# Optimization experiments

Hardware: AMD Instinct MI355X
Metric: run time of the kernel (lower is better)

Reference implementation:

```python
import jax, jax.numpy as jnp
import numpy as np

L, E, D, H, HD, DFF = 15, 1024, 1024, 32, 32, 1536
SC, SH, SG, SEQ, B = 32, 256, 256, 64, 128
ALPHA = (2.0 * L) ** (-0.25)


def setup_inputs() -> dict:
    keys = iter(jax.random.split(jax.random.key(0), 40))
    def rn(shape, s=0.02):
        return jax.random.normal(next(keys), shape, jnp.float32) * s
    inp = {"x": jax.random.normal(next(keys), (B, SEQ, E), jnp.float32)}
    inp.update(
        wq_w=rn((L, E, D)), wq_b=rn((L, D)),
        wk_w=rn((L, E, D)), wk_b=rn((L, D)),
        wv_w=rn((L, E, D)), wv_b=rn((L, D)),
        wo_w=rn((L, D, E)), wo_b=rn((L, E)),
        sc_w=rn((L, E, SC)),
        sh1_w=rn((L, SEQ * SC, SH)), sh1_b=rn((L, SH)),
        sln1_g=jnp.ones((L, SH)), sln1_b=jnp.zeros((L, SH)),
        sgf_w=rn((L, SH, H * SG)), sgf_b=rn((L, H * SG)),
        sln2_g=jnp.ones((L, H * SG)), sln2_b=jnp.zeros((L, H * SG)),
        swg_w=rn((L, SG, SEQ * SEQ)),
        ffn1_w=rn((L, E, DFF)), ffn1_b=rn((L, DFF)),
        ffn2_w=rn((L, DFF, E)), ffn2_b=rn((L, E)),
        n1_g=jnp.ones((L, E)), n1_b=jnp.zeros((L, E)),
        n2_g=jnp.ones((L, E)), n2_b=jnp.zeros((L, E)),
    )
    return inp


def _ln(x, g, b, eps=1e-3):
    m = jnp.mean(x, -1, keepdims=True)
    v = jnp.mean((x - m) ** 2, -1, keepdims=True)
    return (x - m) * jax.lax.rsqrt(v + eps) * g + b


def _mish(x):
    return x * jnp.tanh(jax.nn.softplus(x))


def _encoder_layer(x, p):
    (wq_w, wq_b, wk_w, wk_b, wv_w, wv_b, wo_w, wo_b, sc_w, sh1_w, sh1_b,
     sln1_g, sln1_b, sgf_w, sgf_b, sln2_g, sln2_b, swg_w,
     ffn1_w, ffn1_b, ffn2_w, ffn2_b, n1_g, n1_b, n2_g, n2_b) = p
    b, l, _ = x.shape
    q = (x @ wq_w + wq_b).reshape(b, l, H, HD)
    k = (x @ wk_w + wk_b).reshape(b, l, H, HD)
    v = (x @ wv_w + wv_b).reshape(b, l, H, HD)
    logits = jnp.einsum('bqhd,bkhd->bhqk', q, k) / jnp.sqrt(jnp.float32(HD))
    # smolgen: dynamic per-head 64x64 bias from compressed board features
    c = (x @ sc_w).reshape(b, l * SC)                       # [B, 2048]
    h = _ln(jax.nn.silu(c @ sh1_w + sh1_b), sln1_g, sln1_b)  # [B, 256]
    g = _ln(jax.nn.silu(h @ sgf_w + sgf_b), sln2_g, sln2_b)  # [B, H*256]
    sw = (g.reshape(b, H, SG) @ swg_w).reshape(b, H, l, l)   # [B, H, 64, 64]
    attn = jax.nn.softmax(logits + sw, axis=-1)
    av = jnp.einsum('bhqk,bkhd->bqhd', attn, v).reshape(b, l, D)
    out1 = _ln(x + (av @ wo_w + wo_b) * ALPHA, n1_g, n1_b)
    f = _mish(out1 @ ffn1_w + ffn1_b) @ ffn2_w + ffn2_b
    return _ln(out1 + f * ALPHA, n2_g, n2_b)


def reference(x, wq_w, wq_b, wk_w, wk_b, wv_w, wv_b, wo_w, wo_b, sc_w,
              sh1_w, sh1_b, sln1_g, sln1_b, sgf_w, sgf_b, sln2_g, sln2_b,
              swg_w, ffn1_w, ffn1_b, ffn2_w, ffn2_b, n1_g, n1_b, n2_g, n2_b):
    params = (wq_w, wq_b, wk_w, wk_b, wv_w, wv_b, wo_w, wo_b, sc_w,
              sh1_w, sh1_b, sln1_g, sln1_b, sgf_w, sgf_b, sln2_g, sln2_b,
              swg_w, ffn1_w, ffn1_b, ffn2_w, ffn2_b, n1_g, n1_b, n2_g, n2_b)
    def body(h, p):
        return _encoder_layer(h, p), None
    out, _ = jax.lax.scan(body, x, params)
    return out
```

## Files before the change

### kernel.cpp

```cpp
#include <hip/hip_runtime.h>
#include <hip/hip_bf16.h>

typedef __attribute__((ext_vector_type(8))) short bf16x8;
typedef __attribute__((ext_vector_type(4))) float f32x4;
typedef __hip_bfloat16 bf16;

#define ALPHA_F 0.42728713f
#define LN_EPS 1e-3f

__device__ __forceinline__ float silu_f(float x) { return x / (1.0f + __expf(-x)); }
__device__ __forceinline__ float mish_f(float x) {
  if (x > 20.0f) return x;
  float t = 1.0f + __expf(x);
  float t2 = t * t;
  return x * (t2 - 1.0f) / (t2 + 1.0f);
}
__device__ __forceinline__ unsigned short f2bfu(float x) {
  bf16 h = __float2bfloat16(x);
  return *(unsigned short*)&h;
}
__device__ __forceinline__ float bfu2f(unsigned short u) {
  unsigned int v = (unsigned int)u << 16;
  return *(float*)&v;
}

#define MFMA16(acc, a, b) \
  (acc) = __builtin_amdgcn_mfma_f32_16x16x32_bf16((a), (b), (acc), 0, 0, 0)

#define GLOAD_LDS16(gp, lp)                                                              \
  __builtin_amdgcn_global_load_lds((__attribute__((address_space(1))) void*)(void*)(gp), \
                                   (__attribute__((address_space(3))) void*)(void*)(lp), \
                                   16, 0, 0)

__global__ __launch_bounds__(1) void sentinel_k(float* __restrict__ o) { o[0] = 1.2345e7f; }

__device__ __forceinline__ void transpose_body(
    int tb, float* tile ,
    const float* wq, const float* wk, const float* wv, const float* wo,
    const float* f1, const float* f2, const float* sgf, const float* swg,
    const float* sh1, const float* scw,
    const float* bq, const float* bk, const float* bv,
    bf16* Wqkv, bf16* Wo, bf16* Wf1, bf16* Wf2, bf16* Wsgf, bf16* Wswg,
    bf16* Wsh1, bf16* Wsc, float* bqkv) {
  if (tb >= 10784) {
    int i = (tb - 10784) * 256 + threadIdx.x;
    if (i < 1024) bqkv[i] = bq[i];
    else if (i < 2048) bqkv[i] = bk[i - 1024];
    else bqkv[i] = bv[i - 2048];
    return;
  }
  const float* W;
  bf16* Wt;
  int K, N, b2;
  if (tb < 3072) {
    int m = tb >> 10;
    W = (m == 0) ? wq : ((m == 1) ? wk : wv);
    Wt = Wqkv + (size_t)m * 1024 * 1024;
    K = 1024; N = 1024; b2 = tb & 1023;
  } else if (tb < 4096)  { W = wo;  Wt = Wo;   K = 1024; N = 1024; b2 = tb - 3072; }
  else if (tb < 5632)    { W = f1;  Wt = Wf1;  K = 1024; N = 1536; b2 = tb - 4096; }
  else if (tb < 7168)    { W = f2;  Wt = Wf2;  K = 1536; N = 1024; b2 = tb - 5632; }
  else if (tb < 9216)    { W = sgf; Wt = Wsgf; K = 256;  N = 8192; b2 = tb - 7168; }
  else if (tb < 10240)   { W = swg; Wt = Wswg; K = 256;  N = 4096; b2 = tb - 9216; }
  else if (tb < 10752)   { W = sh1; Wt = Wsh1; K = 2048; N = 256;  b2 = tb - 10240; }
  else                   { W = scw; Wt = Wsc;  K = 1024; N = 32;   b2 = tb - 10752; }
  int ntx = N >> 5;
  int ty_ = b2 / ntx, tx_ = b2 - ty_ * ntx;
  int nb = tx_ * 32, kb = ty_ * 32;
  int tx = threadIdx.x & 31, ty = threadIdx.x >> 5;
#pragma unroll
  for (int i = 0; i < 4; ++i)
    tile[(ty + i * 8) * 33 + tx] = W[(size_t)(kb + ty + i * 8) * N + nb + tx];
  __syncthreads();
#pragma unroll
  for (int i = 0; i < 4; ++i)
    Wt[(size_t)(nb + ty + i * 8) * K + kb + tx] = __float2bfloat16(tile[tx * 33 + ty + i * 8]);
}

__global__ __launch_bounds__(256) void transpose_layer(
    const float* wq, const float* wk, const float* wv, const float* wo,
    const float* f1, const float* f2, const float* sgf, const float* swg,
    const float* sh1, const float* scw,
    const float* bq, const float* bk, const float* bv,
    bf16* Wqkv, bf16* Wo, bf16* Wf1, bf16* Wf2, bf16* Wsgf, bf16* Wswg,
    bf16* Wsh1, bf16* Wsc, float* bqkv) {
  __shared__ float tile[32 * 33];
  transpose_body(blockIdx.x, tile, wq, wk, wv, wo, f1, f2, sgf, swg, sh1, scw,
                 bq, bk, bv, Wqkv, Wo, Wf1, Wf2, Wsgf, Wswg, Wsh1, Wsc, bqkv);
}

__global__ __launch_bounds__(256) void cvt_f32_bf16_k(const float* __restrict__ in,
                                                      bf16* __restrict__ out, long long n) {
  long long i = ((long long)blockIdx.x * 256 + threadIdx.x) * 4;
  if (i + 3 < n) {
    float4 v = *(const float4*)(in + i);
    out[i + 0] = __float2bfloat16(v.x);
    out[i + 1] = __float2bfloat16(v.y);
    out[i + 2] = __float2bfloat16(v.z);
    out[i + 3] = __float2bfloat16(v.w);
  }
}

__global__ __launch_bounds__(256) void megaA(
    const bf16* __restrict__ xb,
    const bf16* __restrict__ Wqkv, const float* __restrict__ bqkv,
    bf16* __restrict__ qkvb,
    const bf16* __restrict__ Wsc, bf16* __restrict__ cbuf,
    int doT,
    const float* wq, const float* wk, const float* wv, const float* wo,
    const float* f1, const float* f2, const float* sgf, const float* swg,
    const float* sh1, const float* scw,
    const float* bq, const float* bk, const float* bv,
    bf16* WqkvN, bf16* WoN, bf16* Wf1N, bf16* Wf2N, bf16* WsgfN, bf16* WswgN,
    bf16* Wsh1N, bf16* WscN, float* bqkvN) {
  __shared__ __align__(128) short LB[16384];
  const int bid = blockIdx.x;
  const int t = threadIdx.x;
  if (bid < 1536) {
    const int lane = t & 63, wave = t >> 6;
    int xcd = bid & 7, lid = bid >> 3;
    int swz = xcd * 192 + lid;
    int by = swz / 24, bx = swz - by * 24;
    int m0 = by << 7, n0 = bx << 7;
    int wr = wave >> 1, wc = wave & 1;
    int fr = lane & 15, fk = (lane >> 4) << 3;
    f32x4 acc[4][4] = {};
    int row0 = t >> 2, ko0 = (t & 3) << 3;
    const bf16* Ag0 = xb + (size_t)(m0 + row0) * 1024 + ko0;
    const bf16* Ag1 = xb + (size_t)(m0 + 64 + row0) * 1024 + ko0;
    const bf16* Bg0 = Wqkv + (size_t)(n0 + row0) * 1024 + ko0;
    const bf16* Bg1 = Wqkv + (size_t)(n0 + 64 + row0) * 1024 + ko0;
    auto stageTo = [&](int buf, int k0) {
      short* Asb = LB + buf * 4096;
      short* Bsb = LB + 8192 + buf * 4096;
      GLOAD_LDS16(Ag0 + k0, Asb + wave * 512);
      GLOAD_LDS16(Ag1 + k0, Asb + 2048 + wave * 512);
      GLOAD_LDS16(Bg0 + k0, Bsb + wave * 512);
      GLOAD_LDS16(Bg1 + k0, Bsb + 2048 + wave * 512);
    };
    stageTo(0, 0);
    __syncthreads();
    const int rdA = (wr * 64 + fr) * 32 + fk;
    const int rdB = (wc * 64 + fr) * 32 + fk;
    for (int kt = 0; kt < 32; ++kt) {
      int cur = kt & 1;
      if (kt + 1 < 32) stageTo(cur ^ 1, (kt + 1) << 5);
      const short* Asb = LB + cur * 4096;
      const short* Bsb = LB + 8192 + cur * 4096;
      bf16x8 af[4], bfv[4];
#pragma unroll
      for (int a = 0; a < 4; ++a) af[a] = *(const bf16x8*)(Asb + rdA + a * 512);
#pragma unroll
      for (int b = 0; b < 4; ++b) bfv[b] = *(const bf16x8*)(Bsb + rdB + b * 512);
#pragma unroll
      for (int a = 0; a < 4; ++a)
#pragma unroll
        for (int b = 0; b < 4; ++b) MFMA16(acc[a][b], af[a], bfv[b]);
      __syncthreads();
    }
    int lr = (lane >> 4) << 2, lc = lane & 15;
#pragma unroll
    for (int a = 0; a < 4; ++a)
#pragma unroll
      for (int b = 0; b < 4; ++b) {
        int col = n0 + wc * 64 + b * 16 + lc;
        float bv = bqkv[col];
#pragma unroll
        for (int j = 0; j < 4; ++j) {
          int rowi = m0 + wr * 64 + a * 16 + lr + j;
          qkvb[(size_t)rowi * 3072 + col] = __float2bfloat16(acc[a][b][j] + bv);
        }
      }
  } else if (bid < 1664) {
    const int lane = t & 63, w = t >> 6;
    const int fr = lane & 15, s4 = lane >> 4;
    const int row0 = ((bid - 1536) * 4 + w) * 16;
    f32x4 acc[2] = {};
    const bf16* Arow = xb + (size_t)(row0 + fr) * 1024 + s4 * 8;
    const bf16* B0 = Wsc + (size_t)fr * 1024 + s4 * 8;
    const bf16* B1 = Wsc + (size_t)(16 + fr) * 1024 + s4 * 8;
#pragma unroll 8
    for (int kt = 0; kt < 32; ++kt) {
      bf16x8 a = *(const bf16x8*)(Arow + kt * 32);
      bf16x8 b0 = *(const bf16x8*)(B0 + kt * 32);
      bf16x8 b1 = *(const bf16x8*)(B1 + kt * 32);
      acc[0] = __builtin_amdgcn_mfma_f32_16x16x32_bf16(a, b0, acc[0], 0, 0, 0);
      acc[1] = __builtin_amdgcn_mfma_f32_16x16x32_bf16(a, b1, acc[1], 0, 0, 0);
    }
#pragma unroll
    for (int n2 = 0; n2 < 2; ++n2)
#pragma unroll
      for (int j = 0; j < 4; ++j)
        cbuf[(size_t)(row0 + s4 * 4 + j) * 32 + n2 * 16 + fr] =
            __float2bfloat16(acc[n2][j]);
  } else {
    if (!doT) return;
    transpose_body(bid - 1664, (float*)LB, wq, wk, wv, wo, f1, f2, sgf, swg, sh1, scw,
                   bq, bk, bv, WqkvN, WoN, Wf1N, Wf2N, WsgfN, WswgN, Wsh1N, WscN, bqkvN);
  }
}

template <int ACT, bool OUTBF16, bool BIAS>
__global__ __launch_bounds__(256) void gemm64b(const bf16* __restrict__ A,
                                               const bf16* __restrict__ Bt,
                                               const float* __restrict__ bias,
                                               float* __restrict__ Cf, bf16* __restrict__ Cb,
                                               int M, int N, int K) {
  __shared__ __align__(128) short As[2 * 4096];
  __shared__ __align__(128) short Bs[2 * 4096];
  int t = threadIdx.x;
  int lane = t & 63, wave = t >> 6;
  int nbx = N >> 6;
  int nwg = gridDim.x;
  int q = nwg >> 3, r = nwg & 7;
  int xcd = blockIdx.x & 7, lid = blockIdx.x >> 3;
  int swz = (xcd < r ? xcd * (q + 1) : r * (q + 1) + (xcd - r) * q) + lid;
  int by = swz / nbx, bx = swz - by * nbx;
  int m0 = by << 6, n0 = bx << 6;
  int fr = lane & 15;
  int fk = (lane >> 4) << 3;

  f32x4 acc[4] = {};

  int row0 = t >> 2, ko0 = (t & 3) << 3;
  const bf16* Ag0 = A + (size_t)(m0 + row0) * K + ko0;
  const bf16* Bg0 = Bt + (size_t)(n0 + row0) * K + ko0;

  auto stageTo = [&](int buf, int k0) {
#pragma unroll
    for (int s = 0; s < 2; ++s) {
      GLOAD_LDS16(Ag0 + k0 + s * 32, As + buf * 4096 + s * 2048 + wave * 512);
      GLOAD_LDS16(Bg0 + k0 + s * 32, Bs + buf * 4096 + s * 2048 + wave * 512);
    }
  };

  int nk = K >> 6;
  stageTo(0, 0);
  __syncthreads();

  const int rdA = (wave * 16 + fr) * 32 + fk;
  const int rdB = fr * 32 + fk;

  for (int kt = 0; kt < nk; ++kt) {
    int cur = kt & 1;
    if (kt + 1 < nk) stageTo(cur ^ 1, (kt + 1) << 6);
    bf16x8 af[2], bfv[4][2];
#pragma unroll
    for (int h = 0; h < 2; ++h) {
      af[h] = *(const bf16x8*)(As + cur * 4096 + h * 2048 + rdA);
#pragma unroll
      for (int b = 0; b < 4; ++b)
        bfv[b][h] = *(const bf16x8*)(Bs + cur * 4096 + h * 2048 + rdB + b * 512);
    }
#pragma unroll
    for (int h = 0; h < 2; ++h)
#pragma unroll
      for (int b = 0; b < 4; ++b) MFMA16(acc[b], af[h], bfv[b][h]);
    __syncthreads();
  }
  int lr = (lane >> 4) << 2;
  int lc = lane & 15;
#pragma unroll
  for (int b = 0; b < 4; ++b) {
    int col = n0 + b * 16 + lc;
    float bv = 0.0f;
    if constexpr (BIAS) bv = bias[col];
#pragma unroll
    for (int j = 0; j < 4; ++j) {
      int rowi = m0 + wave * 16 + lr + j;
      float v = acc[b][j] + bv;
      if constexpr (ACT == 1) v = silu_f(v);
      if constexpr (ACT == 2) v = mish_f(v);
      if constexpr (OUTBF16) Cb[(size_t)rowi * N + col] = __float2bfloat16(v);
      else Cf[(size_t)rowi * N + col] = v;
    }
  }
}

template <int ACT>
__global__ __launch_bounds__(64) void gemm_wave16(const bf16* __restrict__ A,
                                                  const bf16* __restrict__ Bt,
                                                  const float* __restrict__ bias,
                                                  float* __restrict__ Cf,
                                                  int N, int K) {
  const int lane = threadIdx.x;
  const int fr = lane & 15, s4 = lane >> 4;
  const int ncols = N >> 4;
  const int rb = blockIdx.x / ncols, cb = blockIdx.x - rb * ncols;
  const int row0 = rb << 4, col0 = cb << 4;
  f32x4 acc = {};
  const bf16* Arow = A + (size_t)(row0 + fr) * K + s4 * 8;
  const bf16* Brow = Bt + (size_t)(col0 + fr) * K + s4 * 8;
  const int nk = K >> 5;
#pragma unroll 8
  for (int kt = 0; kt < nk; ++kt) {
    bf16x8 a = *(const bf16x8*)(Arow + kt * 32);
    bf16x8 b = *(const bf16x8*)(Brow + kt * 32);
    acc = __builtin_amdgcn_mfma_f32_16x16x32_bf16(a, b, acc, 0, 0, 0);
  }
#pragma unroll
  for (int j = 0; j < 4; ++j) {
    int col = col0 + fr;
    float v = acc[j] + bias[col];
    if constexpr (ACT == 1) v = silu_f(v);
    Cf[(size_t)(row0 + s4 * 4 + j) * N + col] = v;
  }
}

__global__ __launch_bounds__(256) void ln256_kernel(const float* __restrict__ hpre,
                                                    const float* __restrict__ gam,
                                                    const float* __restrict__ bet,
                                                    bf16* __restrict__ hb) {
  __shared__ float rsm[4], rs2[4], st2[2];
  int t = threadIdx.x, row = blockIdx.x;
  float sv = hpre[(size_t)row * 256 + t];
  float s = sv, s2 = sv * sv;
#pragma unroll
  for (int o = 32; o > 0; o >>= 1) { s += __shfl_down(s, o); s2 += __shfl_down(s2, o); }
  if ((t & 63) == 0) { rsm[t >> 6] = s; rs2[t >> 6] = s2; }
  __syncthreads();
  if (t == 0) {
    float a = rsm[0] + rsm[1] + rsm[2] + rsm[3];
    float b2 = rs2[0] + rs2[1] + rs2[2] + rs2[3];
    float m = a * (1.0f / 256.0f);
    st2[0] = m;
    st2[1] = rsqrtf(b2 * (1.0f / 256.0f) - m * m + LN_EPS);
  }
  __syncthreads();
  float y = (sv - st2[0]) * st2[1] * gam[t] + bet[t];
  hb[(size_t)row * 256 + t] = __float2bfloat16(y);
}

__global__ __launch_bounds__(1024) void ln8192_kernel(const float* __restrict__ gpre,
                                                      const float* __restrict__ gam,
                                                      const float* __restrict__ bet,
                                                      bf16* __restrict__ gb) {
  __shared__ float rsm[16], rs2[16], st2[2];
  int t = threadIdx.x, row = blockIdx.x;
  const float* p = gpre + (size_t)row * 8192;
  float v[8];
  float s = 0.0f, s2 = 0.0f;
#pragma unroll
  for (int i = 0; i < 8; ++i) {
    v[i] = p[t + i * 1024];
    s += v[i];
    s2 += v[i] * v[i];
  }
#pragma unroll
  for (int o = 32; o > 0; o >>= 1) { s += __shfl_down(s, o); s2 += __shfl_down(s2, o); }
  int lane = t & 63, w = t >> 6;
  if (lane == 0) { rsm[w] = s; rs2[w] = s2; }
  __syncthreads();
  if (t == 0) {
    float a = 0.0f, b2 = 0.0f;
#pragma unroll
    for (int i = 0; i < 16; ++i) { a += rsm[i]; b2 += rs2[i]; }
    float m = a * (1.0f / 8192.0f);
    st2[0] = m;
    st2[1] = rsqrtf(b2 * (1.0f / 8192.0f) - m * m + LN_EPS);
  }
  __syncthreads();
  float m = st2[0], r = st2[1];
#pragma unroll
  for (int i = 0; i < 8; ++i) {
    int n = t + i * 1024;
    gb[(size_t)row * 8192 + n] = __float2bfloat16((v[i] - m) * r * gam[n] + bet[n]);
  }
}

__global__ __launch_bounds__(256) void ln_residual_kernel(const float* __restrict__ base,
                                                          const bf16* __restrict__ delta,
                                                          const float* __restrict__ gam,
                                                          const float* __restrict__ bet,
                                                          float* __restrict__ outf,
                                                          bf16* __restrict__ outb) {
  __shared__ float rsm[4], rs2[4], st2[2];
  int t = threadIdx.x, row = blockIdx.x;
  float4 bv = ((const float4*)(base + (size_t)row * 1024))[t];
  ushort4 du = ((const ushort4*)(delta + (size_t)row * 1024))[t];
  float4 v;
  v.x = bv.x + bfu2f(du.x) * ALPHA_F;
  v.y = bv.y + bfu2f(du.y) * ALPHA_F;
  v.z = bv.z + bfu2f(du.z) * ALPHA_F;
  v.w = bv.w + bfu2f(du.w) * ALPHA_F;
  float s = v.x + v.y + v.z + v.w;
  float s2 = v.x * v.x + v.y * v.y + v.z * v.z + v.w * v.w;
#pragma unroll
  for (int o = 32; o > 0; o >>= 1) { s += __shfl_down(s, o); s2 += __shfl_down(s2, o); }
  if ((t & 63) == 0) { rsm[t >> 6] = s; rs2[t >> 6] = s2; }
  __syncthreads();
  if (t == 0) {
    float a = rsm[0] + rsm[1] + rsm[2] + rsm[3];
    float b2 = rs2[0] + rs2[1] + rs2[2] + rs2[3];
    float m = a * (1.0f / 1024.0f);
    st2[0] = m;
    st2[1] = rsqrtf(b2 * (1.0f / 1024.0f) - m * m + LN_EPS);
  }
  __syncthreads();
  float m = st2[0], r = st2[1];
  float4 g4 = ((const float4*)gam)[t];
  float4 b4 = ((const float4*)bet)[t];
  float4 y;
  y.x = (v.x - m) * r * g4.x + b4.x;
  y.y = (v.y - m) * r * g4.y + b4.y;
  y.z = (v.z - m) * r * g4.z + b4.z;
  y.w = (v.w - m) * r * g4.w + b4.w;
  ((float4*)(outf + (size_t)row * 1024))[t] = y;
  ushort4 o4;
  o4.x = f2bfu(y.x); o4.y = f2bfu(y.y); o4.z = f2bfu(y.z); o4.w = f2bfu(y.w);
  ((ushort4*)(outb + (size_t)row * 1024))[t] = o4;
}

__global__ __launch_bounds__(256) void attn_kernel(const bf16* __restrict__ qkv,
                                                   const bf16* __restrict__ sw,
                                                   bf16* __restrict__ avb) {
  __shared__ __align__(16) short Vt[32 * 72];
  __shared__ __align__(16) short Pl[64 * 72];
  const int t = threadIdx.x, lane = t & 63, w = t >> 6;
  const int fr = lane & 15, s4 = lane >> 4;
  const int bh = blockIdx.x, b = bh >> 5, h = bh & 31;
  const size_t qb = (size_t)b * 64 * 3072 + h * 32;
  {
    int k = t >> 2, d0 = (t & 3) * 8;
    bf16x8 v = *(const bf16x8*)(qkv + qb + (size_t)k * 3072 + 2048 + d0);
#pragma unroll
    for (int i = 0; i < 8; ++i) Vt[(d0 + i) * 72 + k] = v[i];
  }
  f32x4 acc[4] = {};
  {
    bf16x8 aq = *(const bf16x8*)(qkv + qb + (size_t)(16 * w + fr) * 3072 + s4 * 8);
#pragma unroll
    for (int n = 0; n < 4; ++n) {
      bf16x8 bk = *(const bf16x8*)(qkv + qb + (size_t)(n * 16 + fr) * 3072 + 1024 + s4 * 8);
      acc[n] = __builtin_amdgcn_mfma_f32_16x16x32_bf16(aq, bk, acc[n], 0, 0, 0);
    }
  }
  const bf16* swp = sw + (size_t)bh * 4096;
  float rinv[4];
#pragma unroll
  for (int j = 0; j < 4; ++j) {
    int q = 16 * w + s4 * 4 + j;
    float pv[4];
    float mx = -1e30f;
#pragma unroll
    for (int n = 0; n < 4; ++n) {
      float v = acc[n][j] * 0.17677669529663687f +
                __bfloat162float(swp[q * 64 + n * 16 + fr]);
      pv[n] = v;
      mx = fmaxf(mx, v);
    }
    mx = fmaxf(mx, __shfl_xor(mx, 1));
    mx = fmaxf(mx, __shfl_xor(mx, 2));
    mx = fmaxf(mx, __shfl_xor(mx, 4));
    mx = fmaxf(mx, __shfl_xor(mx, 8));
    float sum = 0.0f;
#pragma unroll
    for (int n = 0; n < 4; ++n) {
      float e = __expf(pv[n] - mx);
      sum += e;
      ((bf16*)Pl)[q * 72 + n * 16 + fr] = __float2bfloat16(e);
    }
    sum += __shfl_xor(sum, 1);
    sum += __shfl_xor(sum, 2);
    sum += __shfl_xor(sum, 4);
    sum += __shfl_xor(sum, 8);
    rinv[j] = 1.0f / sum;
  }
  __syncthreads();
  f32x4 acc2[2] = {};
#pragma unroll
  for (int kt = 0; kt < 2; ++kt) {
    bf16x8 ap = *(const bf16x8*)(Pl + (16 * w + fr) * 72 + kt * 32 + s4 * 8);
#pragma unroll
    for (int n2 = 0; n2 < 2; ++n2) {
      bf16x8 bv = *(const bf16x8*)(Vt + (n2 * 16 + fr) * 72 + kt * 32 + s4 * 8);
      acc2[n2] = __builtin_amdgcn_mfma_f32_16x16x32_bf16(ap, bv, acc2[n2], 0, 0, 0);
    }
  }
#pragma unroll
  for (int n2 = 0; n2 < 2; ++n2) {
#pragma unroll
    for (int j = 0; j < 4; ++j) {
      int q = 16 * w + s4 * 4 + j;
      int d = n2 * 16 + fr;
      avb[(size_t)(b * 64 + q) * 1024 + h * 32 + d] =
          __float2bfloat16(acc2[n2][j] * rinv[j]);
    }
  }
}

extern "C" void kernel_launch(void* const* d_in, const int* in_sizes, int n_in,
                              void* d_out, int out_size, void* d_ws, size_t ws_size,
                              hipStream_t stream) {
  const float* x_in   = (const float*)d_in[0];
  const float* wq_w   = (const float*)d_in[1];
  const float* wq_b   = (const float*)d_in[2];
  const float* wk_w   = (const float*)d_in[3];
  const float* wk_b   = (const float*)d_in[4];
  const float* wv_w   = (const float*)d_in[5];
  const float* wv_b   = (const float*)d_in[6];
  const float* wo_w   = (const float*)d_in[7];
  const float* wo_b   = (const float*)d_in[8];
  const float* sc_w   = (const float*)d_in[9];
  const float* sh1_w  = (const float*)d_in[10];
  const float* sh1_b  = (const float*)d_in[11];
  const float* sln1_g = (const float*)d_in[12];
  const float* sln1_b = (const float*)d_in[13];
  const float* sgf_w  = (const float*)d_in[14];
  const float* sgf_b  = (const float*)d_in[15];
  const float* sln2_g = (const float*)d_in[16];
  const float* sln2_b = (const float*)d_in[17];
  const float* swg_w  = (const float*)d_in[18];
  const float* ffn1_w = (const float*)d_in[19];
  const float* ffn1_b = (const float*)d_in[20];
  const float* ffn2_w = (const float*)d_in[21];
  const float* ffn2_b = (const float*)d_in[22];
  const float* n1_g   = (const float*)d_in[23];
  const float* n1_b   = (const float*)d_in[24];
  const float* n2_g   = (const float*)d_in[25];
  const float* n2_b   = (const float*)d_in[26];

  char* ws = (char*)d_ws;
  size_t off = 0;
  auto alloc = [&](size_t bytes) -> void* {
    void* p = ws + off;
    off += (bytes + 255) & ~(size_t)255;
    return p;
  };
  bf16*  xb    = (bf16*)alloc(8192ULL * 1024 * 2);
  float* P0    = (float*)alloc(8192ULL * 1024 * 4);
  float* P1    = (float*)alloc(8192ULL * 1024 * 4);
  bf16*  dT    = (bf16*)alloc(8192ULL * 1024 * 2);
  bf16*  WqkvB = (bf16*)alloc(2ULL * 3072 * 1024 * 2);
  float* bqkvB = (float*)alloc(2ULL * 3072 * 4);
  bf16*  WoB   = (bf16*)alloc(2ULL * 1024 * 1024 * 2);
  bf16*  Wf1B  = (bf16*)alloc(2ULL * 1536 * 1024 * 2);
  bf16*  Wf2B  = (bf16*)alloc(2ULL * 1024 * 1536 * 2);
  bf16*  WsgfB = (bf16*)alloc(2ULL * 8192 * 256 * 2);
  bf16*  WswgB = (bf16*)alloc(2ULL * 4096 * 256 * 2);
  bf16*  Wsh1B = (bf16*)alloc(2ULL * 256 * 2048 * 2);
  bf16*  WscB  = (bf16*)alloc(2ULL * 32 * 1024 * 2);
  bf16*  qkvb  = (bf16*)alloc(8192ULL * 3072 * 2);
  bf16*  cbuf  = (bf16*)alloc(8192ULL * 32 * 2);
  float* hpre  = (float*)alloc(128ULL * 256 * 4);
  bf16*  hbb   = (bf16*)alloc(128ULL * 256 * 2);
  float* gpre  = (float*)alloc(128ULL * 8192 * 4);
  bf16*  gbb   = (bf16*)alloc(128ULL * 8192 * 2);
  bf16*  swb   = (bf16*)alloc(4096ULL * 4096 * 2);
  bf16*  avb   = (bf16*)alloc(8192ULL * 1024 * 2);
  bf16*  out1b = (bf16*)alloc(8192ULL * 1024 * 2);
  bf16*  f1b   = (bf16*)alloc(8192ULL * 1536 * 2);
  if (off > ws_size) {
    sentinel_k<<<1, 1, 0, stream>>>((float*)d_out);
    return;
  }

  cvt_f32_bf16_k<<<8192, 256, 0, stream>>>(x_in, xb, 8192LL * 1024);
  transpose_layer<<<10796, 256, 0, stream>>>(
      wq_w, wk_w, wv_w, wo_w, ffn1_w, ffn2_w, sgf_w, swg_w, sh1_w, sc_w,
      wq_b, wk_b, wv_b,
      WqkvB, WoB, Wf1B, Wf2B, WsgfB, WswgB, Wsh1B, WscB, bqkvB);

  for (int l = 0; l < 15; ++l) {
    const int cur = l & 1, nxt = cur ^ 1;
    const int lp = l + 1;
    bf16*  Wqkv = WqkvB + (size_t)cur * 3072 * 1024;
    float* bqkv = bqkvB + (size_t)cur * 3072;
    bf16*  Wo   = WoB   + (size_t)cur * 1024 * 1024;
    bf16*  Wf1  = Wf1B  + (size_t)cur * 1536 * 1024;
    bf16*  Wf2  = Wf2B  + (size_t)cur * 1024 * 1536;
    bf16*  Wsgf = WsgfB + (size_t)cur * 8192 * 256;
    bf16*  Wswg = WswgB + (size_t)cur * 4096 * 256;
    bf16*  Wsh1 = Wsh1B + (size_t)cur * 256 * 2048;
    bf16*  Wsc  = WscB  + (size_t)cur * 32 * 1024;

    const float* xc = (l == 0) ? x_in : ((l & 1) ? P0 : P1);
    float* Pout = (l & 1) ? P1 : P0;

    megaA<<<12460, 256, 0, stream>>>(
        xb, Wqkv, bqkv, qkvb, Wsc, cbuf, (l < 14) ? 1 : 0,
        wq_w + (size_t)lp * 1048576, wk_w + (size_t)lp * 1048576,
        wv_w + (size_t)lp * 1048576, wo_w + (size_t)lp * 1048576,
        ffn1_w + (size_t)lp * 1024 * 1536, ffn2_w + (size_t)lp * 1536 * 1024,
        sgf_w + (size_t)lp * 256 * 8192, swg_w + (size_t)lp * 256 * 4096,
        sh1_w + (size_t)lp * 2048 * 256, sc_w + (size_t)lp * 1024 * 32,
        wq_b + (size_t)lp * 1024, wk_b + (size_t)lp * 1024, wv_b + (size_t)lp * 1024,
        WqkvB + (size_t)nxt * 3072 * 1024, WoB + (size_t)nxt * 1024 * 1024,
        Wf1B + (size_t)nxt * 1536 * 1024, Wf2B + (size_t)nxt * 1024 * 1536,
        WsgfB + (size_t)nxt * 8192 * 256, WswgB + (size_t)nxt * 4096 * 256,
        Wsh1B + (size_t)nxt * 256 * 2048, WscB + (size_t)nxt * 32 * 1024,
        bqkvB + (size_t)nxt * 3072);
    gemm_wave16<1><<<128, 64, 0, stream>>>(cbuf, Wsh1, sh1_b + l * 256, hpre, 256, 2048);
    ln256_kernel<<<128, 256, 0, stream>>>(hpre, sln1_g + l * 256, sln1_b + l * 256, hbb);
    gemm_wave16<1><<<4096, 64, 0, stream>>>(hbb, Wsgf, sgf_b + (size_t)l * 8192, gpre,
                                            8192, 256);
    ln8192_kernel<<<128, 1024, 0, stream>>>(gpre, sln2_g + (size_t)l * 8192,
                                            sln2_b + (size_t)l * 8192, gbb);
    gemm64b<0, true, false><<<4096, 256, 0, stream>>>(gbb, Wswg, nullptr, nullptr,
                                                      swb, 4096, 4096, 256);
    attn_kernel<<<4096, 256, 0, stream>>>(qkvb, swb, avb);
    gemm64b<0, true, true><<<2048, 256, 0, stream>>>(avb, Wo, wo_b + l * 1024,
                                                     nullptr, dT, 8192, 1024, 1024);
    ln_residual_kernel<<<8192, 256, 0, stream>>>(xc, dT, n1_g + l * 1024, n1_b + l * 1024,
                                                 Pout, out1b);
    gemm64b<2, true, true><<<3072, 256, 0, stream>>>(out1b, Wf1, ffn1_b + l * 1536,
                                                     nullptr, f1b, 8192, 1536, 1024);
    gemm64b<0, true, true><<<2048, 256, 0, stream>>>(f1b, Wf2, ffn2_b + l * 1024,
                                                     nullptr, dT, 8192, 1024, 1536);
    float* xnext = (l == 14) ? (float*)d_out : Pout;
    ln_residual_kernel<<<8192, 256, 0, stream>>>(Pout, dT, n2_g + l * 1024, n2_b + l * 1024,
                                                 xnext, xb);
  }
}
```

Measured before the change: 5.192 ms.

## Replace double-buffered LDS staging with single-buffer load-sync-compute in GEMM kernels

```diff
diff --git a/kernel.cpp b/kernel.cpp
--- a/kernel.cpp
+++ b/kernel.cpp
@@ -113,7 +113,7 @@
     const float* bq, const float* bk, const float* bv,
     bf16* WqkvN, bf16* WoN, bf16* Wf1N, bf16* Wf2N, bf16* WsgfN, bf16* WswgN,
     bf16* Wsh1N, bf16* WscN, float* bqkvN) {
-  __shared__ __align__(128) short LB[16384];
+  __shared__ __align__(128) short LB[8192];
   const int bid = blockIdx.x;
   const int t = threadIdx.x;
   if (bid < 1536) {
@@ -130,28 +130,20 @@
     const bf16* Ag1 = xb + (size_t)(m0 + 64 + row0) * 1024 + ko0;
     const bf16* Bg0 = Wqkv + (size_t)(n0 + row0) * 1024 + ko0;
     const bf16* Bg1 = Wqkv + (size_t)(n0 + 64 + row0) * 1024 + ko0;
-    auto stageTo = [&](int buf, int k0) {
-      short* Asb = LB + buf * 4096;
-      short* Bsb = LB + 8192 + buf * 4096;
-      GLOAD_LDS16(Ag0 + k0, Asb + wave * 512);
-      GLOAD_LDS16(Ag1 + k0, Asb + 2048 + wave * 512);
-      GLOAD_LDS16(Bg0 + k0, Bsb + wave * 512);
-      GLOAD_LDS16(Bg1 + k0, Bsb + 2048 + wave * 512);
-    };
-    stageTo(0, 0);
-    __syncthreads();
     const int rdA = (wr * 64 + fr) * 32 + fk;
-    const int rdB = (wc * 64 + fr) * 32 + fk;
+    const int rdB = 4096 + (wc * 64 + fr) * 32 + fk;
     for (int kt = 0; kt < 32; ++kt) {
-      int cur = kt & 1;
-      if (kt + 1 < 32) stageTo(cur ^ 1, (kt + 1) << 5);
-      const short* Asb = LB + cur * 4096;
-      const short* Bsb = LB + 8192 + cur * 4096;
+      int k0 = kt << 5;
+      GLOAD_LDS16(Ag0 + k0, LB + wave * 512);
+      GLOAD_LDS16(Ag1 + k0, LB + 2048 + wave * 512);
+      GLOAD_LDS16(Bg0 + k0, LB + 4096 + wave * 512);
+      GLOAD_LDS16(Bg1 + k0, LB + 6144 + wave * 512);
+      __syncthreads();
       bf16x8 af[4], bfv[4];
 #pragma unroll
-      for (int a = 0; a < 4; ++a) af[a] = *(const bf16x8*)(Asb + rdA + a * 512);
-#pragma unroll
-      for (int b = 0; b < 4; ++b) bfv[b] = *(const bf16x8*)(Bsb + rdB + b * 512);
+      for (int a = 0; a < 4; ++a) af[a] = *(const bf16x8*)(LB + rdA + a * 512);
+#pragma unroll
+      for (int b = 0; b < 4; ++b) bfv[b] = *(const bf16x8*)(LB + rdB + b * 512);
 #pragma unroll
       for (int a = 0; a < 4; ++a)
 #pragma unroll
@@ -206,8 +198,8 @@
                                                const float* __restrict__ bias,
                                                float* __restrict__ Cf, bf16* __restrict__ Cb,
                                                int M, int N, int K) {
-  __shared__ __align__(128) short As[2 * 4096];
-  __shared__ __align__(128) short Bs[2 * 4096];
+  __shared__ __align__(128) short As[4096];
+  __shared__ __align__(128) short Bs[4096];
   int t = threadIdx.x;
   int lane = t & 63, wave = t >> 6;
   int nbx = N >> 6;
@@ -226,31 +218,25 @@
   const bf16* Ag0 = A + (size_t)(m0 + row0) * K + ko0;
   const bf16* Bg0 = Bt + (size_t)(n0 + row0) * K + ko0;
 
-  auto stageTo = [&](int buf, int k0) {
-#pragma unroll
-    for (int s = 0; s < 2; ++s) {
-      GLOAD_LDS16(Ag0 + k0 + s * 32, As + buf * 4096 + s * 2048 + wave * 512);
-      GLOAD_LDS16(Bg0 + k0 + s * 32, Bs + buf * 4096 + s * 2048 + wave * 512);
-    }
-  };
-
   int nk = K >> 6;
-  stageTo(0, 0);
-  __syncthreads();
-
   const int rdA = (wave * 16 + fr) * 32 + fk;
   const int rdB = fr * 32 + fk;
 
   for (int kt = 0; kt < nk; ++kt) {
-    int cur = kt & 1;
-    if (kt + 1 < nk) stageTo(cur ^ 1, (kt + 1) << 6);
+    int k0 = kt << 6;
+#pragma unroll
+    for (int s = 0; s < 2; ++s) {
+      GLOAD_LDS16(Ag0 + k0 + s * 32, As + s * 2048 + wave * 512);
+      GLOAD_LDS16(Bg0 + k0 + s * 32, Bs + s * 2048 + wave * 512);
+    }
+    __syncthreads();
     bf16x8 af[2], bfv[4][2];
 #pragma unroll
     for (int h = 0; h < 2; ++h) {
-      af[h] = *(const bf16x8*)(As + cur * 4096 + h * 2048 + rdA);
+      af[h] = *(const bf16x8*)(As + h * 2048 + rdA);
 #pragma unroll
       for (int b = 0; b < 4; ++b)
-        bfv[b][h] = *(const bf16x8*)(Bs + cur * 4096 + h * 2048 + rdB + b * 512);
+        bfv[b][h] = *(const bf16x8*)(Bs + h * 2048 + rdB + b * 512);
     }
 #pragma unroll
     for (int h = 0; h < 2; ++h)
```

Result: faster. 5.069 ms (median of 2 runs) (-2.4%).
